# Kernel optimization log

Hardware: AMD Instinct MI355X
Metric: run time of the kernel (lower is better)

The kernel has to match this reference:

```python
import math
import jax, jax.numpy as jnp
import numpy as np

IN_DIM = 1024
OUT_DIM = 1024
K = 32
N_BANDS = 3
TOTAL_K = K * N_BANDS
LAYER_IDX = 0
NUM_LAYERS = 1
SCALE = math.sqrt(2.0 / (IN_DIM + OUT_DIM))


def _make_pos():
    l_val = (LAYER_IDX + 1) / (NUM_LAYERS + 1)
    i_idx = (jnp.arange(IN_DIM, dtype=jnp.float32) + 1) / (IN_DIM + 1)
    j_idx = (jnp.arange(OUT_DIM, dtype=jnp.float32) + 1) / (OUT_DIM + 1)
    ii, jj = jnp.meshgrid(i_idx, j_idx, indexing='ij')
    pos = jnp.stack([ii, jj, jnp.full_like(ii, l_val)], axis=-1)
    return pos.reshape(-1, 3)  # (in_dim*out_dim, 3)


def setup_inputs() -> dict:
    key = jax.random.key(0)
    kx, ko, kp, ka = jax.random.split(key, 4)
    x = jax.random.normal(kx, (4096, IN_DIM), dtype=jnp.float32)
    # omega with per-band scaling (1 + band*3), matching the torch init
    band_scales = jnp.repeat(1.0 + 3.0 * jnp.arange(N_BANDS, dtype=jnp.float32), K)
    omega = jax.random.normal(ko, (TOTAL_K, 3), dtype=jnp.float32) * band_scales[:, None]
    phi = jax.random.normal(kp, (TOTAL_K,), dtype=jnp.float32) * math.pi
    alpha = jax.random.normal(ka, (2 * TOTAL_K,), dtype=jnp.float32) * 0.01 / (1.0 + jnp.arange(2 * TOTAL_K, dtype=jnp.float32))
    bias = jnp.zeros((OUT_DIM,), dtype=jnp.float32)
    pos = _make_pos()
    return {"x": x, "omega": omega, "phi": phi, "alpha": alpha, "bias": bias, "pos": pos}


def reference(x, omega, phi, alpha, bias, pos):
    # args: (in*out, total_k)
    args = pos @ omega.T + phi
    # features @ alpha == sin(args)@alpha[:K2//2] + cos(args)@alpha[K2//2:]
    a_sin, a_cos = alpha[:TOTAL_K], alpha[TOTAL_K:]
    w_flat = jnp.sin(args) @ a_sin + jnp.cos(args) @ a_cos  # (in*out,)
    # torch: w = flat.reshape(in, out).T * scale; F.linear(x, w) = x @ w.T
    w_t = w_flat.reshape(IN_DIM, OUT_DIM) * SCALE  # == w.T
    return x @ w_t + bias
```

## Files before the change

kernel.cpp:

```cpp
#include <hip/hip_runtime.h>
#include <hip/hip_bf16.h>
#include <math.h>


#define IN_DIM   1024
#define OUT_DIM  1024
#define NBANDS   96
#define KTAB     192
#define MX       4096
#define SCALE_W  0.03125f
#define NSPLIT   4

typedef __bf16 bf16x8 __attribute__((ext_vector_type(8)));
typedef float  f32x4  __attribute__((ext_vector_type(4)));

#define AS1 __attribute__((address_space(1)))
#define AS3 __attribute__((address_space(3)))

__device__ __forceinline__ void gload_lds16(const void* g, void* l) {
  __builtin_amdgcn_global_load_lds((AS1 void*)(g), (AS3 void*)(l), 16, 0, 0);
}

__device__ __forceinline__ unsigned short bf16bits(float f) {
  __hip_bfloat16 b = __float2bfloat16(f);
  return *(unsigned short*)&b;
}

__global__ void build_tables(const float* __restrict__ omega,
                             const float* __restrict__ phi,
                             const float* __restrict__ alpha,
                             __hip_bfloat16* __restrict__ TaT,
                             __hip_bfloat16* __restrict__ Tb) {
  const int t = blockIdx.x;
  const int i = blockIdx.y * 256 + threadIdx.x;
  const float ox = omega[3 * t], oy = omega[3 * t + 1], oz = omega[3 * t + 2];
  const float uc = oz * 0.5f + phi[t];
  const float as_ = alpha[t], ac = alpha[NBANDS + t];
  const float coord = (float)(i + 1) / 1025.0f;
  float su, cu;
  sincosf(ox * coord + uc, &su, &cu);
  TaT[(size_t)(2 * t) * IN_DIM + i]     = __float2bfloat16(SCALE_W * (as_ * su + ac * cu));
  TaT[(size_t)(2 * t + 1) * IN_DIM + i] = __float2bfloat16(SCALE_W * (as_ * cu - ac * su));
  float sv, cv;
  sincosf(oy * coord, &sv, &cv);
  Tb[(size_t)i * KTAB + 2 * t]     = __float2bfloat16(cv);
  Tb[(size_t)i * KTAB + 2 * t + 1] = __float2bfloat16(sv);
}

__global__ __launch_bounds__(256)
void gemm_xta(const float* __restrict__ X,
              const __hip_bfloat16* __restrict__ TaT,
              float* __restrict__ Pp) {
  __shared__ __align__(16) __hip_bfloat16 As[2][32 * 64];
  __shared__ __align__(16) __hip_bfloat16 Bs[2][192 * 64];
  const int tid  = threadIdx.x;
  const int lane = tid & 63;
  const int wc   = tid >> 6;
  const int m0   = blockIdx.y * 32;
  const int ks0  = blockIdx.z * (IN_DIM / NSPLIT);
  const int lr = lane & 15;
  const int lk = (lane >> 4) * 8;

  const float* xbase = X + (size_t)m0 * IN_DIM + ks0;
  const __hip_bfloat16* bbase = TaT + ks0;

  f32x4 acc[2][3] = {};

  auto ALOAD = [&](int t, float4* a) {
#pragma unroll
    for (int q = 0; q < 2; ++q) {
      const int f = q * 256 + tid;
      const int r = f >> 4, c4 = f & 15;
      a[q] = *(const float4*)(xbase + (size_t)r * IN_DIM + t * 64 + c4 * 4);
    }
  };
  auto AWRITE = [&](int buf, const float4* a) {
#pragma unroll
    for (int q = 0; q < 2; ++q) {
      const int f = q * 256 + tid;
      const int r = f >> 4, c4 = f & 15;
      ushort4 o;
      o.x = bf16bits(a[q].x); o.y = bf16bits(a[q].y);
      o.z = bf16bits(a[q].z); o.w = bf16bits(a[q].w);
      *(ushort4*)((char*)&As[buf][0] + r * 128 + c4 * 8) = o;
    }
  };
  auto BSTAGE = [&](int t, int buf) {
#pragma unroll
    for (int q = 0; q < 6; ++q) {
      const int f = q * 256 + tid;
      const int r = f >> 3, g = f & 7;
      gload_lds16(bbase + (size_t)r * IN_DIM + t * 64 + g * 8,
                  (char*)&Bs[buf][0] + (size_t)f * 16);
    }
  };
  auto COMPUTE = [&](int buf) {
#pragma unroll
    for (int kk = 0; kk < 2; ++kk) {
      bf16x8 af[2], bfr[3];
#pragma unroll
      for (int mi = 0; mi < 2; ++mi)
        af[mi] = *(const bf16x8*)&As[buf][(mi * 16 + lr) * 64 + kk * 32 + lk];
#pragma unroll
      for (int ni = 0; ni < 3; ++ni)
        bfr[ni] = *(const bf16x8*)&Bs[buf][(wc * 48 + ni * 16 + lr) * 64 + kk * 32 + lk];
#pragma unroll
      for (int mi = 0; mi < 2; ++mi)
#pragma unroll
        for (int ni = 0; ni < 3; ++ni)
          acc[mi][ni] = __builtin_amdgcn_mfma_f32_16x16x32_bf16(
              af[mi], bfr[ni], acc[mi][ni], 0, 0, 0);
    }
  };

  float4 a0[2];
  ALOAD(0, a0); BSTAGE(0, 0); AWRITE(0, a0);
  __syncthreads();
#pragma unroll
  for (int t = 0; t < 4; ++t) {
    const int cur = t & 1;
    float4 an[2];
    if (t < 3) { ALOAD(t + 1, an); BSTAGE(t + 1, cur ^ 1); }
    COMPUTE(cur);
    if (t < 3) AWRITE(cur ^ 1, an);
    __syncthreads();
  }

  float* P = Pp + (size_t)blockIdx.z * (MX * KTAB);
#pragma unroll
  for (int mi = 0; mi < 2; ++mi)
#pragma unroll
    for (int ni = 0; ni < 3; ++ni)
#pragma unroll
      for (int r = 0; r < 4; ++r) {
        const int row = m0 + mi * 16 + (lane >> 4) * 4 + r;
        const int col = wc * 48 + ni * 16 + lr;
        P[(size_t)row * KTAB + col] = acc[mi][ni][r];
      }
}

__global__ void reduce_y(const float* __restrict__ Pp,
                         __hip_bfloat16* __restrict__ Y) {
  const int i = (blockIdx.x * 256 + threadIdx.x) * 4;
  const int S = MX * KTAB;
  float4 a = *(const float4*)(Pp + i);
  float4 b = *(const float4*)(Pp + S + i);
  float4 c = *(const float4*)(Pp + 2 * S + i);
  float4 d = *(const float4*)(Pp + 3 * S + i);
  ushort4 o;
  o.x = bf16bits(a.x + b.x + c.x + d.x);
  o.y = bf16bits(a.y + b.y + c.y + d.y);
  o.z = bf16bits(a.z + b.z + c.z + d.z);
  o.w = bf16bits(a.w + b.w + c.w + d.w);
  *(ushort4*)(Y + i) = o;
}

__global__ __launch_bounds__(256)
void gemm_out(const __hip_bfloat16* __restrict__ Y,
              const __hip_bfloat16* __restrict__ Tb,
              float* __restrict__ out,
              const float* __restrict__ bias) {
  __shared__ __align__(16) __hip_bfloat16 As[2][64 * 64];
  __shared__ __align__(16) __hip_bfloat16 Bs[2][128 * 64];
  const int tid  = threadIdx.x;
  const int lane = tid & 63;
  const int wave = tid >> 6;
  const int wr = wave >> 1;
  const int wc = wave & 1;
  const int m0 = blockIdx.y * 64;
  const int n0 = blockIdx.x * 128;
  const int lr = lane & 15;
  const int lk = (lane >> 4) * 8;

  f32x4 acc[2][4] = {};

  auto ASTAGE = [&](int t, int buf) {
#pragma unroll
    for (int q = 0; q < 2; ++q) {
      const int f = q * 256 + tid;
      const int r = f >> 3, g = f & 7;
      gload_lds16(Y + (size_t)(m0 + r) * KTAB + t * 64 + g * 8,
                  (char*)&As[buf][0] + (size_t)f * 16);
    }
  };
  auto BSTAGE = [&](int t, int buf) {
#pragma unroll
    for (int q = 0; q < 4; ++q) {
      const int f = q * 256 + tid;
      const int r = f >> 3, g = f & 7;
      gload_lds16(Tb + (size_t)(n0 + r) * KTAB + t * 64 + g * 8,
                  (char*)&Bs[buf][0] + (size_t)f * 16);
    }
  };
  auto COMPUTE = [&](int buf) {
#pragma unroll
    for (int kk = 0; kk < 2; ++kk) {
      bf16x8 af[2], bfr[4];
#pragma unroll
      for (int mi = 0; mi < 2; ++mi)
        af[mi] = *(const bf16x8*)&As[buf][(wr * 32 + mi * 16 + lr) * 64 + kk * 32 + lk];
#pragma unroll
      for (int ni = 0; ni < 4; ++ni)
        bfr[ni] = *(const bf16x8*)&Bs[buf][(wc * 64 + ni * 16 + lr) * 64 + kk * 32 + lk];
#pragma unroll
      for (int mi = 0; mi < 2; ++mi)
#pragma unroll
        for (int ni = 0; ni < 4; ++ni)
          acc[mi][ni] = __builtin_amdgcn_mfma_f32_16x16x32_bf16(
              af[mi], bfr[ni], acc[mi][ni], 0, 0, 0);
    }
  };

  ASTAGE(0, 0); BSTAGE(0, 0);
  __syncthreads();
#pragma unroll
  for (int t = 0; t < 3; ++t) {
    const int cur = t & 1;
    if (t < 2) { ASTAGE(t + 1, cur ^ 1); BSTAGE(t + 1, cur ^ 1); }
    COMPUTE(cur);
    __syncthreads();
  }

#pragma unroll
  for (int mi = 0; mi < 2; ++mi)
#pragma unroll
    for (int ni = 0; ni < 4; ++ni)
#pragma unroll
      for (int r = 0; r < 4; ++r) {
        const int row = m0 + wr * 32 + mi * 16 + (lane >> 4) * 4 + r;
        const int col = n0 + wc * 64 + ni * 16 + lr;
        out[(size_t)row * OUT_DIM + col] = acc[mi][ni][r] + bias[col];
      }
}

extern "C" void kernel_launch(void* const* d_in, const int* in_sizes, int n_in,
                              void* d_out, int out_size, void* d_ws, size_t ws_size,
                              hipStream_t stream) {
  const float* x     = (const float*)d_in[0];
  const float* omega = (const float*)d_in[1];
  const float* phi   = (const float*)d_in[2];
  const float* alpha = (const float*)d_in[3];
  const float* bias  = (const float*)d_in[4];
  float* out = (float*)d_out;
  (void)in_sizes; (void)n_in; (void)out_size; (void)ws_size;

  char* ws = (char*)d_ws;
  float* Pp           = (float*)(ws);
  __hip_bfloat16* Y   = (__hip_bfloat16*)(ws + 12582912);
  __hip_bfloat16* TaT = (__hip_bfloat16*)(ws + 14155776);
  __hip_bfloat16* Tb  = (__hip_bfloat16*)(ws + 14548992);

  build_tables<<<dim3(NBANDS, 4), dim3(256), 0, stream>>>(omega, phi, alpha, TaT, Tb);
  gemm_xta<<<dim3(1, MX / 32, NSPLIT), dim3(256), 0, stream>>>(x, TaT, Pp);
  reduce_y<<<dim3((MX * KTAB) / (256 * 4)), dim3(256), 0, stream>>>(Pp, Y);
  gemm_out<<<dim3(OUT_DIM / 128, MX / 64), dim3(256), 0, stream>>>(Y, Tb, out, bias);
}
```

Baseline: 99.03 us.

## Drop split-K partials and reduce kernel; swizzle LDS layouts in both GEMMs

The first GEMM no longer splits K four ways. It uses 16-row tiles over the full K with 256 blocks and writes bf16 Y directly, which removes the fp32 partial buffer and the separate reduce kernel along with one launch. Both GEMMs also XOR-swizzle their LDS layouts, applied on the global-to-LDS load addresses and on the fragment reads, to avoid bank conflicts. The trade-off is a longer serial K loop per block, with 16 stages, and the TaT table reloaded by 256 blocks.

```diff
diff --git a/kernel.cpp b/kernel.cpp
--- a/kernel.cpp
+++ b/kernel.cpp
@@ -9,7 +9,6 @@
 #define KTAB     192
 #define MX       4096
 #define SCALE_W  0.03125f
-#define NSPLIT   4
 
 typedef __bf16 bf16x8 __attribute__((ext_vector_type(8)));
 typedef float  f32x4  __attribute__((ext_vector_type(4)));
@@ -50,109 +49,81 @@
 __global__ __launch_bounds__(256)
 void gemm_xta(const float* __restrict__ X,
               const __hip_bfloat16* __restrict__ TaT,
-              float* __restrict__ Pp) {
-  __shared__ __align__(16) __hip_bfloat16 As[2][32 * 64];
+              __hip_bfloat16* __restrict__ Y) {
+  __shared__ __align__(16) __hip_bfloat16 As[2][16 * 64];
   __shared__ __align__(16) __hip_bfloat16 Bs[2][192 * 64];
   const int tid  = threadIdx.x;
   const int lane = tid & 63;
   const int wc   = tid >> 6;
-  const int m0   = blockIdx.y * 32;
-  const int ks0  = blockIdx.z * (IN_DIM / NSPLIT);
+  const int m0   = blockIdx.x * 16;
   const int lr = lane & 15;
-  const int lk = (lane >> 4) * 8;
-
-  const float* xbase = X + (size_t)m0 * IN_DIM + ks0;
-  const __hip_bfloat16* bbase = TaT + ks0;
-
-  f32x4 acc[2][3] = {};
-
-  auto ALOAD = [&](int t, float4* a) {
-#pragma unroll
-    for (int q = 0; q < 2; ++q) {
-      const int f = q * 256 + tid;
-      const int r = f >> 4, c4 = f & 15;
-      a[q] = *(const float4*)(xbase + (size_t)r * IN_DIM + t * 64 + c4 * 4);
-    }
-  };
-  auto AWRITE = [&](int buf, const float4* a) {
-#pragma unroll
-    for (int q = 0; q < 2; ++q) {
-      const int f = q * 256 + tid;
-      const int r = f >> 4, c4 = f & 15;
-      ushort4 o;
-      o.x = bf16bits(a[q].x); o.y = bf16bits(a[q].y);
-      o.z = bf16bits(a[q].z); o.w = bf16bits(a[q].w);
-      *(ushort4*)((char*)&As[buf][0] + r * 128 + c4 * 8) = o;
-    }
+  const int hi = lane >> 4;
+
+  const float* xbase = X + (size_t)m0 * IN_DIM;
+
+  f32x4 acc[3] = {};
+
+  auto ALOAD = [&](int t, float4& a) {
+    const int r = tid >> 4, c4 = tid & 15;
+    a = *(const float4*)(xbase + (size_t)r * IN_DIM + t * 64 + c4 * 4);
+  };
+  auto AWRITE = [&](int buf, const float4& a) {
+    const int r = tid >> 4, c4 = tid & 15;
+    ushort4 o;
+    o.x = bf16bits(a.x); o.y = bf16bits(a.y);
+    o.z = bf16bits(a.z); o.w = bf16bits(a.w);
+    const int byte = r * 128 + ((((c4 >> 1) ^ (r & 7)) << 4) | ((c4 & 1) << 3));
+    *(ushort4*)((char*)&As[buf][0] + byte) = o;
   };
   auto BSTAGE = [&](int t, int buf) {
 #pragma unroll
     for (int q = 0; q < 6; ++q) {
       const int f = q * 256 + tid;
       const int r = f >> 3, g = f & 7;
-      gload_lds16(bbase + (size_t)r * IN_DIM + t * 64 + g * 8,
+      gload_lds16(TaT + (size_t)r * IN_DIM + t * 64 + ((g ^ (r & 7)) * 8),
                   (char*)&Bs[buf][0] + (size_t)f * 16);
     }
   };
   auto COMPUTE = [&](int buf) {
 #pragma unroll
     for (int kk = 0; kk < 2; ++kk) {
-      bf16x8 af[2], bfr[3];
-#pragma unroll
-      for (int mi = 0; mi < 2; ++mi)
-        af[mi] = *(const bf16x8*)&As[buf][(mi * 16 + lr) * 64 + kk * 32 + lk];
+      bf16x8 af, bfr[3];
+      af = *(const bf16x8*)((char*)&As[buf][0] +
+            lr * 128 + (((kk * 4 + hi) ^ (lr & 7)) << 4));
+#pragma unroll
+      for (int ni = 0; ni < 3; ++ni) {
+        const int row = wc * 48 + ni * 16 + lr;
+        bfr[ni] = *(const bf16x8*)((char*)&Bs[buf][0] +
+                   row * 128 + (((kk * 4 + hi) ^ (row & 7)) << 4));
+      }
 #pragma unroll
       for (int ni = 0; ni < 3; ++ni)
-        bfr[ni] = *(const bf16x8*)&Bs[buf][(wc * 48 + ni * 16 + lr) * 64 + kk * 32 + lk];
-#pragma unroll
-      for (int mi = 0; mi < 2; ++mi)
-#pragma unroll
-        for (int ni = 0; ni < 3; ++ni)
-          acc[mi][ni] = __builtin_amdgcn_mfma_f32_16x16x32_bf16(
-              af[mi], bfr[ni], acc[mi][ni], 0, 0, 0);
-    }
-  };
-
-  float4 a0[2];
+        acc[ni] = __builtin_amdgcn_mfma_f32_16x16x32_bf16(
+            af, bfr[ni], acc[ni], 0, 0, 0);
+    }
+  };
+
+  float4 a0;
   ALOAD(0, a0); BSTAGE(0, 0); AWRITE(0, a0);
   __syncthreads();
 #pragma unroll
-  for (int t = 0; t < 4; ++t) {
+  for (int t = 0; t < 16; ++t) {
     const int cur = t & 1;
-    float4 an[2];
-    if (t < 3) { ALOAD(t + 1, an); BSTAGE(t + 1, cur ^ 1); }
+    float4 an;
+    if (t < 15) { ALOAD(t + 1, an); BSTAGE(t + 1, cur ^ 1); }
     COMPUTE(cur);
-    if (t < 3) AWRITE(cur ^ 1, an);
+    if (t < 15) AWRITE(cur ^ 1, an);
     __syncthreads();
   }
 
-  float* P = Pp + (size_t)blockIdx.z * (MX * KTAB);
-#pragma unroll
-  for (int mi = 0; mi < 2; ++mi)
-#pragma unroll
-    for (int ni = 0; ni < 3; ++ni)
-#pragma unroll
-      for (int r = 0; r < 4; ++r) {
-        const int row = m0 + mi * 16 + (lane >> 4) * 4 + r;
-        const int col = wc * 48 + ni * 16 + lr;
-        P[(size_t)row * KTAB + col] = acc[mi][ni][r];
-      }
-}
-
-__global__ void reduce_y(const float* __restrict__ Pp,
-                         __hip_bfloat16* __restrict__ Y) {
-  const int i = (blockIdx.x * 256 + threadIdx.x) * 4;
-  const int S = MX * KTAB;
-  float4 a = *(const float4*)(Pp + i);
-  float4 b = *(const float4*)(Pp + S + i);
-  float4 c = *(const float4*)(Pp + 2 * S + i);
-  float4 d = *(const float4*)(Pp + 3 * S + i);
-  ushort4 o;
-  o.x = bf16bits(a.x + b.x + c.x + d.x);
-  o.y = bf16bits(a.y + b.y + c.y + d.y);
-  o.z = bf16bits(a.z + b.z + c.z + d.z);
-  o.w = bf16bits(a.w + b.w + c.w + d.w);
-  *(ushort4*)(Y + i) = o;
+#pragma unroll
+  for (int ni = 0; ni < 3; ++ni)
+#pragma unroll
+    for (int r = 0; r < 4; ++r) {
+      const int row = m0 + hi * 4 + r;
+      const int col = wc * 48 + ni * 16 + lr;
+      Y[(size_t)row * KTAB + col] = __float2bfloat16(acc[ni][r]);
+    }
 }
 
 __global__ __launch_bounds__(256)
@@ -170,7 +141,7 @@
   const int m0 = blockIdx.y * 64;
   const int n0 = blockIdx.x * 128;
   const int lr = lane & 15;
-  const int lk = (lane >> 4) * 8;
+  const int hi = lane >> 4;
 
   f32x4 acc[2][4] = {};
 
@@ -179,7 +150,7 @@
     for (int q = 0; q < 2; ++q) {
       const int f = q * 256 + tid;
       const int r = f >> 3, g = f & 7;
-      gload_lds16(Y + (size_t)(m0 + r) * KTAB + t * 64 + g * 8,
+      gload_lds16(Y + (size_t)(m0 + r) * KTAB + t * 64 + ((g ^ (r & 7)) * 8),
                   (char*)&As[buf][0] + (size_t)f * 16);
     }
   };
@@ -188,7 +159,7 @@
     for (int q = 0; q < 4; ++q) {
       const int f = q * 256 + tid;
       const int r = f >> 3, g = f & 7;
-      gload_lds16(Tb + (size_t)(n0 + r) * KTAB + t * 64 + g * 8,
+      gload_lds16(Tb + (size_t)(n0 + r) * KTAB + t * 64 + ((g ^ (r & 7)) * 8),
                   (char*)&Bs[buf][0] + (size_t)f * 16);
     }
   };
@@ -197,11 +168,17 @@
     for (int kk = 0; kk < 2; ++kk) {
       bf16x8 af[2], bfr[4];
 #pragma unroll
-      for (int mi = 0; mi < 2; ++mi)
-        af[mi] = *(const bf16x8*)&As[buf][(wr * 32 + mi * 16 + lr) * 64 + kk * 32 + lk];
-#pragma unroll
-      for (int ni = 0; ni < 4; ++ni)
-        bfr[ni] = *(const bf16x8*)&Bs[buf][(wc * 64 + ni * 16 + lr) * 64 + kk * 32 + lk];
+      for (int mi = 0; mi < 2; ++mi) {
+        const int row = wr * 32 + mi * 16 + lr;
+        af[mi] = *(const bf16x8*)((char*)&As[buf][0] +
+                  row * 128 + (((kk * 4 + hi) ^ (row & 7)) << 4));
+      }
+#pragma unroll
+      for (int ni = 0; ni < 4; ++ni) {
+        const int row = wc * 64 + ni * 16 + lr;
+        bfr[ni] = *(const bf16x8*)((char*)&Bs[buf][0] +
+                   row * 128 + (((kk * 4 + hi) ^ (row & 7)) << 4));
+      }
 #pragma unroll
       for (int mi = 0; mi < 2; ++mi)
 #pragma unroll
@@ -227,7 +204,7 @@
     for (int ni = 0; ni < 4; ++ni)
 #pragma unroll
       for (int r = 0; r < 4; ++r) {
-        const int row = m0 + wr * 32 + mi * 16 + (lane >> 4) * 4 + r;
+        const int row = m0 + wr * 32 + mi * 16 + hi * 4 + r;
         const int col = n0 + wc * 64 + ni * 16 + lr;
         out[(size_t)row * OUT_DIM + col] = acc[mi][ni][r] + bias[col];
       }
@@ -245,13 +222,11 @@
   (void)in_sizes; (void)n_in; (void)out_size; (void)ws_size;
 
   char* ws = (char*)d_ws;
-  float* Pp           = (float*)(ws);
-  __hip_bfloat16* Y   = (__hip_bfloat16*)(ws + 12582912);
-  __hip_bfloat16* TaT = (__hip_bfloat16*)(ws + 14155776);
-  __hip_bfloat16* Tb  = (__hip_bfloat16*)(ws + 14548992);
+  __hip_bfloat16* Y   = (__hip_bfloat16*)(ws);
+  __hip_bfloat16* TaT = (__hip_bfloat16*)(ws + 1572864);
+  __hip_bfloat16* Tb  = (__hip_bfloat16*)(ws + 1966080);
 
   build_tables<<<dim3(NBANDS, 4), dim3(256), 0, stream>>>(omega, phi, alpha, TaT, Tb);
-  gemm_xta<<<dim3(1, MX / 32, NSPLIT), dim3(256), 0, stream>>>(x, TaT, Pp);
-  reduce_y<<<dim3((MX * KTAB) / (256 * 4)), dim3(256), 0, stream>>>(Pp, Y);
+  gemm_xta<<<dim3(MX / 16), dim3(256), 0, stream>>>(x, TaT, Y);
   gemm_out<<<dim3(OUT_DIM / 128, MX / 64), dim3(256), 0, stream>>>(Y, Tb, out, bias);
 }
```

Measured after the change: 100.8 us. About the same (+1.8%).
